# Kernel tuning notes

Measured on AMD Instinct MI355X. Metric: run time of the kernel, lower is better.

The kernel has to match this reference:

```python
import jax, jax.numpy as jnp
import numpy as np

B, N, H = 4, 200, 300


def setup_inputs() -> dict:
    key = jax.random.key(0)
    ks = jax.random.split(key, 6)
    s = 1.0 / np.sqrt(H)
    return {
        "x": jax.random.normal(ks[0], (B, N, H), dtype=jnp.float32),
        "e": jax.random.normal(ks[1], (B, N, N, H), dtype=jnp.float32),
        "U_w": jax.random.uniform(ks[2], (H, H), jnp.float32, -s, s),
        "U_b": jax.random.uniform(ks[3], (H,), jnp.float32, -s, s),
        "V_w": jax.random.uniform(ks[4], (H, H), jnp.float32, -s, s),
        "V_b": jax.random.uniform(ks[5], (H,), jnp.float32, -s, s),
    }


def reference(x, e, U_w, U_b, V_w, V_b):
    # Ue = e @ U_w.T + U_b  -> (B, N, N, H)
    Ue = jnp.einsum("bijh,gh->bijg", e, U_w) + U_b
    # Vx = x @ V_w.T + V_b  -> (B, N, H)
    Vx = jnp.einsum("bnh,gh->bng", x, V_w) + V_b
    # e_new[b,i,j] = Ue[b,i,j] + Vx[b,i] + Vx[b,j]
    e_new = Ue + Vx[:, :, None, :] + Vx[:, None, :, :]
    return e_new
```

## Files before the change

### kernel.cpp

```cpp
#include <hip/hip_runtime.h>
#include <hip/hip_bf16.h>

#define BB 4
#define NN 200
#define HH 300
#define KSN 10
#define GHF 10
#define NTH 5000
#define SLOTS 1024
#define BHALF_BYTES (KSN * GHF * 1024)

typedef __attribute__((ext_vector_type(8))) short short8;
typedef __attribute__((ext_vector_type(4))) float float4v;

static __device__ __forceinline__ ushort f2bf(float x) {
    union { float f; uint u; } v; v.f = x;
    uint r = v.u + 0x7FFFu + ((v.u >> 16) & 1u);
    return (ushort)(r >> 16);
}

static __device__ __forceinline__ short8 pack8_cvt(float4v a, float4v b) {
    uint u0, u1, u2, u3;
    asm("v_cvt_pk_bf16_f32 %0, %1, %2" : "=v"(u0) : "v"(a[0]), "v"(a[1]));
    asm("v_cvt_pk_bf16_f32 %0, %1, %2" : "=v"(u1) : "v"(a[2]), "v"(a[3]));
    asm("v_cvt_pk_bf16_f32 %0, %1, %2" : "=v"(u2) : "v"(b[0]), "v"(b[1]));
    asm("v_cvt_pk_bf16_f32 %0, %1, %2" : "=v"(u3) : "v"(b[2]), "v"(b[3]));
    union { uint u[4]; short8 s; } r;
    r.u[0] = u0; r.u[1] = u1; r.u[2] = u2; r.u[3] = u3;
    return r.s;
}

static __device__ __forceinline__ void gload_lds16(const void* g, void* l) {
    __builtin_amdgcn_global_load_lds(
        (const __attribute__((address_space(1))) unsigned int*)g,
        (__attribute__((address_space(3))) unsigned int*)l, 16, 0, 0);
}

__global__ void pack_u(const float* __restrict__ Uw, ushort* __restrict__ Bp) {
    int idx = blockIdx.x * 256 + threadIdx.x;
    if (idx >= 2 * KSN * GHF * 64) return;
    int lane = idx & 63;
    int rem = idx >> 6;
    int fh = rem % GHF;
    int ks = (rem / GHF) % KSN;
    int gh = rem / (GHF * KSN);
    int g = (gh * GHF + fh) * 16 + (lane & 15);
    int h0 = ks * 32 + (lane >> 4) * 8;
    ushort v[8];
#pragma unroll
    for (int j = 0; j < 8; ++j) {
        int h = h0 + j;
        v[j] = (g < HH && h < HH) ? f2bf(Uw[g * HH + h]) : (ushort)0;
    }
    *reinterpret_cast<short8*>(Bp + (size_t)idx * 8) = *reinterpret_cast<const short8*>(v);
}

__global__ void vx_kernel(const float* __restrict__ x, const float* __restrict__ Vw,
                          const float* __restrict__ Vb, const float* __restrict__ Ub,
                          float* __restrict__ Vx) {
    __shared__ float xs[HH];
    int row = blockIdx.x;
    const float* xr = x + (size_t)row * HH;
    for (int h = threadIdx.x; h < HH; h += 256) xs[h] = xr[h];
    __syncthreads();
    for (int g = threadIdx.x; g < HH; g += 256) {
        const float4* wr = reinterpret_cast<const float4*>(Vw + (size_t)g * HH);
        const float4* xv = reinterpret_cast<const float4*>(xs);
        float s0 = 0.f, s1 = 0.f, s2 = 0.f, s3 = 0.f;
#pragma unroll 5
        for (int k = 0; k < HH / 4; ++k) {
            float4 w = wr[k];
            float4 xx = xv[k];
            s0 += w.x * xx.x; s1 += w.y * xx.y; s2 += w.z * xx.z; s3 += w.w * xx.w;
        }
        Vx[(size_t)row * HH + g] = Vb[g] + 0.5f * Ub[g] + s0 + s1 + s2 + s3;
    }
}

__launch_bounds__(512, 2)
__global__ void gemm_kernel(const float* __restrict__ e, const ushort* __restrict__ Bp,
                            const float* __restrict__ Vx, float* __restrict__ out) {
    __shared__ ushort Blds[BHALF_BYTES / 2];
    const int tid = threadIdx.x;
    const int lane = tid & 63, wave = tid >> 6;
    const int gh = blockIdx.x >> 7;
    const int bslot = blockIdx.x & 127;
    const int slot = bslot * 8 + wave;
    const int r = lane & 15, q = lane >> 4;
    const int kq = q * 8;

    const char* bsrc = (const char*)Bp + (size_t)gh * BHALF_BYTES;
#pragma unroll
    for (int i = 0; i < 13; ++i) {
        int off = i * 8192 + tid * 16;
        if (off < BHALF_BYTES)
            gload_lds16(bsrc + off, (char*)Blds + off);
    }

    int T = slot;
    const float* rowA = e + (size_t)(T * 32 + r) * HH;
    const float* rowB = rowA + 16 * HH;

#define LOADSET(PA0, PA1, PB0, PB1, RA_, RB_, KS_) do {                        \
        int c0_ = (KS_) * 32 + kq;                                             \
        const float* p0_ = (c0_ + 4 <= HH) ? (RA_) + c0_ : e;                  \
        const float* p1_ = (c0_ + 8 <= HH) ? (RA_) + c0_ + 4 : e;              \
        const float* p2_ = (c0_ + 4 <= HH) ? (RB_) + c0_ : e;                  \
        const float* p3_ = (c0_ + 8 <= HH) ? (RB_) + c0_ + 4 : e;              \
        PA0 = *reinterpret_cast<const float4v*>(p0_);                          \
        PA1 = *reinterpret_cast<const float4v*>(p1_);                          \
        PB0 = *reinterpret_cast<const float4v*>(p2_);                          \
        PB1 = *reinterpret_cast<const float4v*>(p3_);                          \
    } while (0)

    float4v s0a0, s0a1, s0b0, s0b1, s1a0, s1a1, s1b0, s1b1,
            s2a0, s2a1, s2b0, s2b1, s3a0, s3a1, s3b0, s3b1,
            s4a0, s4a1, s4b0, s4b1;

    LOADSET(s0a0, s0a1, s0b0, s0b1, rowA, rowB, 0);
    LOADSET(s1a0, s1a1, s1b0, s1b1, rowA, rowB, 1);
    LOADSET(s2a0, s2a1, s2b0, s2b1, rowA, rowB, 2);
    LOADSET(s3a0, s3a1, s3b0, s3b1, rowA, rowB, 3);
    LOADSET(s4a0, s4a1, s4b0, s4b1, rowA, rowB, 4);

    asm volatile("s_waitcnt vmcnt(0)" ::: "memory");
    __syncthreads();

#define BODY(KS_, SA0, SA1, SB0, SB1, RA_, RB_, PKS_) do {                     \
        short8 fa_ = pack8_cvt(SA0, SA1);                                      \
        short8 fb_ = pack8_cvt(SB0, SB1);                                      \
        LOADSET(SA0, SA1, SB0, SB1, RA_, RB_, PKS_);                           \
        const ushort* bb_ = Blds + (KS_) * (GHF * 512) + lane * 8;             \
        _Pragma("unroll")                                                      \
        for (int f_ = 0; f_ < GHF; ++f_) {                                     \
            short8 bf_ = *reinterpret_cast<const short8*>(bb_ + f_ * 512);     \
            acc0[f_] = __builtin_amdgcn_mfma_f32_16x16x32_bf16(bf_, fa_, acc0[f_], 0, 0, 0); \
            acc1[f_] = __builtin_amdgcn_mfma_f32_16x16x32_bf16(bf_, fb_, acc1[f_], 0, 0, 0); \
        }                                                                      \
    } while (0)

#pragma unroll 1
    for (int it = 0; it < 5; ++it) {
        if (T >= NTH) break;
        int Tn = T + SLOTS;
        int Tc = (Tn < NTH) ? Tn : 0;
        const float* rowAn = e + (size_t)(Tc * 32 + r) * HH;
        const float* rowBn = rowAn + 16 * HH;

        float4v acc0[GHF], acc1[GHF];
#pragma unroll
        for (int f = 0; f < GHF; ++f) {
            acc0[f] = (float4v){0.f, 0.f, 0.f, 0.f};
            acc1[f] = (float4v){0.f, 0.f, 0.f, 0.f};
        }

        BODY(0, s0a0, s0a1, s0b0, s0b1, rowA,  rowB,  5);
        BODY(1, s1a0, s1a1, s1b0, s1b1, rowA,  rowB,  6);
        BODY(2, s2a0, s2a1, s2b0, s2b1, rowA,  rowB,  7);
        BODY(3, s3a0, s3a1, s3b0, s3b1, rowA,  rowB,  8);
        BODY(4, s4a0, s4a1, s4b0, s4b1, rowA,  rowB,  9);
        BODY(5, s0a0, s0a1, s0b0, s0b1, rowAn, rowBn, 0);
        BODY(6, s1a0, s1a1, s1b0, s1b1, rowAn, rowBn, 1);
        BODY(7, s2a0, s2a1, s2b0, s2b1, rowAn, rowBn, 2);
        BODY(8, s3a0, s3a1, s3b0, s3b1, rowAn, rowBn, 3);
        BODY(9, s4a0, s4a1, s4b0, s4b1, rowAn, rowBn, 4);

        const int gb = gh * (GHF * 16);
#pragma unroll
        for (int t2 = 0; t2 < 2; ++t2) {
            int m = T * 32 + t2 * 16 + r;
            int j = m % NN;
            int ti = m / NN;
            int b = ti / NN;
            const float* vi = Vx + (size_t)ti * HH;
            const float* vj = Vx + (size_t)(b * NN + j) * HH;
            float* orow = out + (size_t)m * HH;
#pragma unroll
            for (int f = 0; f < GHF; ++f) {
                int g0 = gb + f * 16 + q * 4;
                if (g0 + 4 <= HH) {
                    float4v v = t2 ? acc1[f] : acc0[f];
                    float4v vi4 = *reinterpret_cast<const float4v*>(vi + g0);
                    float4v vj4 = *reinterpret_cast<const float4v*>(vj + g0);
                    *reinterpret_cast<float4v*>(orow + g0) = v + vi4 + vj4;
                }
            }
        }

        T = Tn;
        rowA = rowAn;
        rowB = rowBn;
    }
#undef BODY
#undef LOADSET
}

extern "C" void kernel_launch(void* const* d_in, const int* in_sizes, int n_in,
                              void* d_out, int out_size, void* d_ws, size_t ws_size,
                              hipStream_t stream) {
    const float* x  = (const float*)d_in[0];
    const float* e  = (const float*)d_in[1];
    const float* Uw = (const float*)d_in[2];
    const float* Ub = (const float*)d_in[3];
    const float* Vw = (const float*)d_in[4];
    const float* Vb = (const float*)d_in[5];
    float* out = (float*)d_out;

    ushort* Bp = (ushort*)d_ws;
    float*  Vx = (float*)((char*)d_ws + 204800);

    pack_u<<<50, 256, 0, stream>>>(Uw, Bp);
    vx_kernel<<<BB * NN, 256, 0, stream>>>(x, Vw, Vb, Ub, Vx);
    gemm_kernel<<<256, 512, 0, stream>>>(e, Bp, Vx, out);
}
```

Measured before the change: 179.8 us.

## Replace persistent LDS-staged GEMM with one-tile-per-wave grid reading B from global

The persistent kernel, where each wave looped over several 32-row tiles using a U-weight half staged in LDS, is replaced by a grid of 2500 blocks of 4 waves. Each wave handles one 32-row tile and one output-column half, reading the packed bf16 weights straight from global or L2 memory. This removes LDS staging, the block-wide barrier and the cross-iteration prefetch of the next tile. In exchange, every wave re-reads B from cache and the A-load prefetch now reaches only one k-chunk ahead. The aim is higher occupancy and better latency hiding through many small waves.

```diff
diff --git a/kernel.cpp b/kernel.cpp
--- a/kernel.cpp
+++ b/kernel.cpp
@@ -4,11 +4,8 @@
 #define BB 4
 #define NN 200
 #define HH 300
-#define KSN 10
+#define NCH 10
 #define GHF 10
-#define NTH 5000
-#define SLOTS 1024
-#define BHALF_BYTES (KSN * GHF * 1024)
 
 typedef __attribute__((ext_vector_type(8))) short short8;
 typedef __attribute__((ext_vector_type(4))) float float4v;
@@ -30,20 +27,14 @@
     return r.s;
 }
 
-static __device__ __forceinline__ void gload_lds16(const void* g, void* l) {
-    __builtin_amdgcn_global_load_lds(
-        (const __attribute__((address_space(1))) unsigned int*)g,
-        (__attribute__((address_space(3))) unsigned int*)l, 16, 0, 0);
-}
-
 __global__ void pack_u(const float* __restrict__ Uw, ushort* __restrict__ Bp) {
     int idx = blockIdx.x * 256 + threadIdx.x;
-    if (idx >= 2 * KSN * GHF * 64) return;
+    if (idx >= 2 * NCH * GHF * 64) return;
     int lane = idx & 63;
     int rem = idx >> 6;
     int fh = rem % GHF;
-    int ks = (rem / GHF) % KSN;
-    int gh = rem / (GHF * KSN);
+    int ks = (rem / GHF) % NCH;
+    int gh = rem / (GHF * NCH);
     int g = (gh * GHF + fh) * 16 + (lane & 15);
     int h0 = ks * 32 + (lane >> 4) * 8;
     ushort v[8];
@@ -77,122 +68,82 @@
     }
 }
 
-__launch_bounds__(512, 2)
+__launch_bounds__(256, 4)
 __global__ void gemm_kernel(const float* __restrict__ e, const ushort* __restrict__ Bp,
                             const float* __restrict__ Vx, float* __restrict__ out) {
-    __shared__ ushort Blds[BHALF_BYTES / 2];
     const int tid = threadIdx.x;
     const int lane = tid & 63, wave = tid >> 6;
-    const int gh = blockIdx.x >> 7;
-    const int bslot = blockIdx.x & 127;
-    const int slot = bslot * 8 + wave;
-    const int r = lane & 15, q = lane >> 4;
-    const int kq = q * 8;
+    const int task = blockIdx.x * 4 + wave;
+    const int gh = task & 1;
+    const int tile = task >> 1;
+    const int m0 = tile * 32;
+    const int r = lane & 15, q = lane >> 4, kq = q * 8;
 
-    const char* bsrc = (const char*)Bp + (size_t)gh * BHALF_BYTES;
+    const float* rowA = e + (size_t)(m0 + r) * HH;
+    const float* rowB = rowA + 16 * HH;
+    const ushort* bb = Bp + (size_t)gh * (NCH * GHF * 512);
+
+    float4v acc0[GHF], acc1[GHF];
 #pragma unroll
-    for (int i = 0; i < 13; ++i) {
-        int off = i * 8192 + tid * 16;
-        if (off < BHALF_BYTES)
-            gload_lds16(bsrc + off, (char*)Blds + off);
+    for (int f = 0; f < GHF; ++f) {
+        acc0[f] = (float4v){0.f, 0.f, 0.f, 0.f};
+        acc1[f] = (float4v){0.f, 0.f, 0.f, 0.f};
     }
 
-    int T = slot;
-    const float* rowA = e + (size_t)(T * 32 + r) * HH;
-    const float* rowB = rowA + 16 * HH;
+    float4v a0, a1, b0, b1;
 
-#define LOADSET(PA0, PA1, PB0, PB1, RA_, RB_, KS_) do {                        \
-        int c0_ = (KS_) * 32 + kq;                                             \
-        const float* p0_ = (c0_ + 4 <= HH) ? (RA_) + c0_ : e;                  \
-        const float* p1_ = (c0_ + 8 <= HH) ? (RA_) + c0_ + 4 : e;              \
-        const float* p2_ = (c0_ + 4 <= HH) ? (RB_) + c0_ : e;                  \
-        const float* p3_ = (c0_ + 8 <= HH) ? (RB_) + c0_ + 4 : e;              \
-        PA0 = *reinterpret_cast<const float4v*>(p0_);                          \
-        PA1 = *reinterpret_cast<const float4v*>(p1_);                          \
-        PB0 = *reinterpret_cast<const float4v*>(p2_);                          \
-        PB1 = *reinterpret_cast<const float4v*>(p3_);                          \
+#define LOAD_A(K_) do {                                                         \
+        int c0_ = (K_) * 32 + kq;                                               \
+        const float* p0_ = (c0_ + 4 <= HH) ? rowA + c0_ : e;                    \
+        const float* p1_ = (c0_ + 8 <= HH) ? rowA + c0_ + 4 : e;                \
+        const float* p2_ = (c0_ + 4 <= HH) ? rowB + c0_ : e;                    \
+        const float* p3_ = (c0_ + 8 <= HH) ? rowB + c0_ + 4 : e;                \
+        a0 = *reinterpret_cast<const float4v*>(p0_);                            \
+        a1 = *reinterpret_cast<const float4v*>(p1_);                            \
+        b0 = *reinterpret_cast<const float4v*>(p2_);                            \
+        b1 = *reinterpret_cast<const float4v*>(p3_);                            \
     } while (0)
 
-    float4v s0a0, s0a1, s0b0, s0b1, s1a0, s1a1, s1b0, s1b1,
-            s2a0, s2a1, s2b0, s2b1, s3a0, s3a1, s3b0, s3b1,
-            s4a0, s4a1, s4b0, s4b1;
-
-    LOADSET(s0a0, s0a1, s0b0, s0b1, rowA, rowB, 0);
-    LOADSET(s1a0, s1a1, s1b0, s1b1, rowA, rowB, 1);
-    LOADSET(s2a0, s2a1, s2b0, s2b1, rowA, rowB, 2);
-    LOADSET(s3a0, s3a1, s3b0, s3b1, rowA, rowB, 3);
-    LOADSET(s4a0, s4a1, s4b0, s4b1, rowA, rowB, 4);
-
-    asm volatile("s_waitcnt vmcnt(0)" ::: "memory");
-    __syncthreads();
-
-#define BODY(KS_, SA0, SA1, SB0, SB1, RA_, RB_, PKS_) do {                     \
-        short8 fa_ = pack8_cvt(SA0, SA1);                                      \
-        short8 fb_ = pack8_cvt(SB0, SB1);                                      \
-        LOADSET(SA0, SA1, SB0, SB1, RA_, RB_, PKS_);                           \
-        const ushort* bb_ = Blds + (KS_) * (GHF * 512) + lane * 8;             \
-        _Pragma("unroll")                                                      \
-        for (int f_ = 0; f_ < GHF; ++f_) {                                     \
-            short8 bf_ = *reinterpret_cast<const short8*>(bb_ + f_ * 512);     \
+#define BODY(KS_) do {                                                          \
+        short8 fa_ = pack8_cvt(a0, a1);                                         \
+        short8 fb_ = pack8_cvt(b0, b1);                                         \
+        if ((KS_) + 1 < NCH) LOAD_A((KS_) + 1);                                 \
+        const ushort* bks_ = bb + (size_t)(KS_) * (GHF * 512) + lane * 8;       \
+        _Pragma("unroll")                                                       \
+        for (int f_ = 0; f_ < GHF; ++f_) {                                      \
+            short8 bf_ = *reinterpret_cast<const short8*>(bks_ + f_ * 512);     \
             acc0[f_] = __builtin_amdgcn_mfma_f32_16x16x32_bf16(bf_, fa_, acc0[f_], 0, 0, 0); \
             acc1[f_] = __builtin_amdgcn_mfma_f32_16x16x32_bf16(bf_, fb_, acc1[f_], 0, 0, 0); \
-        }                                                                      \
+        }                                                                       \
     } while (0)
 
-#pragma unroll 1
-    for (int it = 0; it < 5; ++it) {
-        if (T >= NTH) break;
-        int Tn = T + SLOTS;
-        int Tc = (Tn < NTH) ? Tn : 0;
-        const float* rowAn = e + (size_t)(Tc * 32 + r) * HH;
-        const float* rowBn = rowAn + 16 * HH;
+    LOAD_A(0);
+    BODY(0); BODY(1); BODY(2); BODY(3); BODY(4);
+    BODY(5); BODY(6); BODY(7); BODY(8); BODY(9);
+#undef BODY
+#undef LOAD_A
 
-        float4v acc0[GHF], acc1[GHF];
+    const int gb = gh * (GHF * 16);
+#pragma unroll
+    for (int t2 = 0; t2 < 2; ++t2) {
+        int m = m0 + t2 * 16 + r;
+        int j = m % NN;
+        int ti = m / NN;
+        int b = ti / NN;
+        const float* vi = Vx + (size_t)ti * HH;
+        const float* vj = Vx + (size_t)(b * NN + j) * HH;
+        float* orow = out + (size_t)m * HH;
 #pragma unroll
         for (int f = 0; f < GHF; ++f) {
-            acc0[f] = (float4v){0.f, 0.f, 0.f, 0.f};
-            acc1[f] = (float4v){0.f, 0.f, 0.f, 0.f};
-        }
-
-        BODY(0, s0a0, s0a1, s0b0, s0b1, rowA,  rowB,  5);
-        BODY(1, s1a0, s1a1, s1b0, s1b1, rowA,  rowB,  6);
-        BODY(2, s2a0, s2a1, s2b0, s2b1, rowA,  rowB,  7);
-        BODY(3, s3a0, s3a1, s3b0, s3b1, rowA,  rowB,  8);
-        BODY(4, s4a0, s4a1, s4b0, s4b1, rowA,  rowB,  9);
-        BODY(5, s0a0, s0a1, s0b0, s0b1, rowAn, rowBn, 0);
-        BODY(6, s1a0, s1a1, s1b0, s1b1, rowAn, rowBn, 1);
-        BODY(7, s2a0, s2a1, s2b0, s2b1, rowAn, rowBn, 2);
-        BODY(8, s3a0, s3a1, s3b0, s3b1, rowAn, rowBn, 3);
-        BODY(9, s4a0, s4a1, s4b0, s4b1, rowAn, rowBn, 4);
-
-        const int gb = gh * (GHF * 16);
-#pragma unroll
-        for (int t2 = 0; t2 < 2; ++t2) {
-            int m = T * 32 + t2 * 16 + r;
-            int j = m % NN;
-            int ti = m / NN;
-            int b = ti / NN;
-            const float* vi = Vx + (size_t)ti * HH;
-            const float* vj = Vx + (size_t)(b * NN + j) * HH;
-            float* orow = out + (size_t)m * HH;
-#pragma unroll
-            for (int f = 0; f < GHF; ++f) {
-                int g0 = gb + f * 16 + q * 4;
-                if (g0 + 4 <= HH) {
-                    float4v v = t2 ? acc1[f] : acc0[f];
-                    float4v vi4 = *reinterpret_cast<const float4v*>(vi + g0);
-                    float4v vj4 = *reinterpret_cast<const float4v*>(vj + g0);
-                    *reinterpret_cast<float4v*>(orow + g0) = v + vi4 + vj4;
-                }
+            int g0 = gb + f * 16 + q * 4;
+            if (g0 + 4 <= HH) {
+                float4v v = t2 ? acc1[f] : acc0[f];
+                float4v vi4 = *reinterpret_cast<const float4v*>(vi + g0);
+                float4v vj4 = *reinterpret_cast<const float4v*>(vj + g0);
+                *reinterpret_cast<float4v*>(orow + g0) = v + vi4 + vj4;
             }
         }
-
-        T = Tn;
-        rowA = rowAn;
-        rowB = rowBn;
     }
-#undef BODY
-#undef LOADSET
 }
 
 extern "C" void kernel_launch(void* const* d_in, const int* in_sizes, int n_in,
@@ -211,5 +162,5 @@
 
     pack_u<<<50, 256, 0, stream>>>(Uw, Bp);
     vx_kernel<<<BB * NN, 256, 0, stream>>>(x, Vw, Vb, Ub, Vx);
-    gemm_kernel<<<256, 512, 0, stream>>>(e, Bp, Vx, out);
+    gemm_kernel<<<2500, 256, 0, stream>>>(e, Bp, Vx, out);
 }
```

New measurement: 262.8 us. +46.2%, slower.
